# Performance work log

Measured on AMD Instinct MI355X. Metric: run time of the kernel, lower is better.

## Reference

```python
import jax, jax.numpy as jnp
import numpy as np

B, S, D, H, M = 4, 4096, 768, 12, 256
Dh = D // H
EPS_KERNEL = 1e-4
LN_EPS = 1e-5


def setup_inputs() -> dict:
    key = jax.random.key(0)
    ks = jax.random.split(key, 18)
    w = lambda k, sh: jax.random.normal(k, sh, jnp.float32) * 0.02
    return {
        "x": jax.random.normal(ks[0], (B, S, D), jnp.float32),
        # FAVOR+ random projection (performer uses orthogonal gaussian; gaussian here, same math)
        "proj": jax.random.normal(ks[1], (M, Dh), jnp.float32),
        "wq": w(ks[2], (D, D)), "bq": jnp.zeros((D,), jnp.float32),
        "wk": w(ks[3], (D, D)), "bk": jnp.zeros((D,), jnp.float32),
        "wv": w(ks[4], (D, D)), "bv": jnp.zeros((D,), jnp.float32),
        "wo": w(ks[5], (D, D)), "bo": jnp.zeros((D,), jnp.float32),
        "ln1_g": jnp.ones((D,), jnp.float32), "ln1_b": jnp.zeros((D,), jnp.float32),
        "ln2_g": jnp.ones((D,), jnp.float32), "ln2_b": jnp.zeros((D,), jnp.float32),
        "w1": w(ks[6], (4 * D, D)), "b1": jnp.zeros((4 * D,), jnp.float32),
        "w2": w(ks[7], (D, 4 * D)), "b2": jnp.zeros((D,), jnp.float32),
    }


def layernorm(x, g, b):
    mu = x.mean(-1, keepdims=True)
    var = ((x - mu) ** 2).mean(-1, keepdims=True)
    return (x - mu) / jnp.sqrt(var + LN_EPS) * g + b


def softmax_features(data, proj, is_query):
    # FAVOR+ positive softmax kernel features (performer-pytorch softmax_kernel)
    norm = data.shape[-1] ** -0.25
    ratio = proj.shape[0] ** -0.5
    dd = jnp.einsum('bhnd,md->bhnm', data * norm, proj)       # [B,H,S,M]
    diag = (data ** 2).sum(-1, keepdims=True) * 0.5 * norm * norm
    if is_query:
        mx = jnp.max(dd, axis=-1, keepdims=True)
    else:
        mx = jnp.max(dd)
    return ratio * (jnp.exp(dd - diag - mx) + EPS_KERNEL)


def performer_block(x, proj, wq, bq, wk, bk, wv, bv, wo, bo,
                    ln1_g, ln1_b, ln2_g, ln2_b, w1, b1, w2, b2):
    h = layernorm(x, ln1_g, ln1_b)
    split = lambda t: t.reshape(B, S, H, Dh).transpose(0, 2, 1, 3)  # [B,H,S,Dh]
    q = split(h @ wq.T + bq)
    k = split(h @ wk.T + bk)
    v = split(h @ wv.T + bv)

    qp = softmax_features(q, proj, True)    # [B,H,S,M]
    kp = softmax_features(k, proj, False)   # [B,H,S,M]

    # non-causal linear attention
    k_sum = kp.sum(axis=2)                                   # [B,H,M]
    d_inv = 1.0 / jnp.einsum('bhnm,bhm->bhn', qp, k_sum)     # [B,H,S]
    ctx = jnp.einsum('bhnm,bhnd->bhmd', kp, v)               # [B,H,M,Dh]
    attn = jnp.einsum('bhnm,bhmd,bhn->bhnd', qp, ctx, d_inv) # [B,H,S,Dh]
    attn = attn.transpose(0, 2, 1, 3).reshape(B, S, D)
    x = x + attn @ wo.T + bo

    h2 = layernorm(x, ln2_g, ln2_b)
    h2 = jax.nn.gelu(h2 @ w1.T + b1, approximate=False)
    x = x + h2 @ w2.T + b2
    return x


def reference(x, proj, wq, bq, wk, bk, wv, bv, wo, bo,
              ln1_g, ln1_b, ln2_g, ln2_b, w1, b1, w2, b2):
    return performer_block(x, proj, wq, bq, wk, bk, wv, bv, wo, bo,
                           ln1_g, ln1_b, ln2_g, ln2_b, w1, b1, w2, b2)
```

## Files before the change

kernel.cpp:

```cpp
#include <hip/hip_runtime.h>
#include <math.h>

typedef __attribute__((ext_vector_type(8))) short bf16x8;
typedef __attribute__((ext_vector_type(4))) float f32x4;

__device__ __forceinline__ float b2f(unsigned short u) {
    return __uint_as_float(((unsigned)u) << 16);
}
__device__ __forceinline__ unsigned short f2b(float f) {
    unsigned u = __float_as_uint(f);
    u += 0x7FFF + ((u >> 16) & 1);
    return (unsigned short)(u >> 16);
}
__device__ __forceinline__ void up2(unsigned u, float& a, float& b) {
    a = __uint_as_float(u << 16);
    b = __uint_as_float(u & 0xffff0000u);
}
__device__ __forceinline__ float gelu_exact(float v) {
    return 0.5f * v * (1.0f + erff(v * 0.70710678118654752f));
}
__device__ __forceinline__ void atomicMaxFloat(float* addr, float val) {
    unsigned* ua = (unsigned*)addr;
    unsigned old = *ua;
    while (true) {
        float of = __uint_as_float(old);
        if (of >= val) break;
        unsigned assumed = old;
        old = atomicCAS(ua, assumed, __float_as_uint(val));
        if (old == assumed) break;
    }
}
__device__ __forceinline__ void gl_lds16(const unsigned short* g, unsigned short* lds) {
    __builtin_amdgcn_global_load_lds((const __attribute__((address_space(1))) unsigned int*)g,
                                     (__attribute__((address_space(3))) unsigned int*)lds, 16, 0, 0);
}

__global__ void init_kernel(float* ksum, float* kmax) {
    int i = blockIdx.x * 256 + threadIdx.x;
    if (i < 48 * 256) ksum[i] = 0.0f;
    if (i == 0) *kmax = -3.0e38f;
}

__global__ __launch_bounds__(256)
void cvt_qkvp(const float* __restrict__ wq, const float* __restrict__ wk, const float* __restrict__ wv,
              const float* __restrict__ prj, unsigned short* __restrict__ wdst,
              unsigned short* __restrict__ pdst) {
    int i4 = (blockIdx.x * 256 + threadIdx.x) * 4;
    const float* s; unsigned short* d; int off;
    if (i4 < 1769472) { s = (i4 < 589824) ? wq : (i4 < 1179648 ? wk : wv);
        off = (i4 < 589824) ? i4 : (i4 < 1179648 ? i4 - 589824 : i4 - 1179648);
        d = wdst + i4; }
    else { s = prj; off = i4 - 1769472; d = pdst + off; }
    float4 v = *(const float4*)&s[off];
    ushort4 o; o.x = f2b(v.x); o.y = f2b(v.y); o.z = f2b(v.z); o.w = f2b(v.w);
    *(ushort4*)d = o;
}
__global__ __launch_bounds__(256)
void cvt_ow12(const float* __restrict__ wo, const float* __restrict__ w1, const float* __restrict__ w2,
              unsigned short* __restrict__ dst) {
    int i4 = (blockIdx.x * 256 + threadIdx.x) * 4;
    const float* s; int off;
    if (i4 < 589824) { s = wo; off = i4; }
    else if (i4 < 2949120) { s = w1; off = i4 - 589824; }
    else { s = w2; off = i4 - 2949120; }
    float4 v = *(const float4*)&s[off];
    ushort4 o; o.x = f2b(v.x); o.y = f2b(v.y); o.z = f2b(v.z); o.w = f2b(v.w);
    *(ushort4*)&dst[i4] = o;
}

template <bool IN_F32>
__global__ __launch_bounds__(256)
void ln_kernel(const void* __restrict__ Xv, const float* __restrict__ G,
               const float* __restrict__ Bb, unsigned short* __restrict__ OUT) {
    int row = blockIdx.x, t = threadIdx.x, wave = t >> 6, lane = t & 63;
    __shared__ float red[4];
    float x0, x1, x2;
    if constexpr (IN_F32) {
        const float* xr = (const float*)Xv + (size_t)row * 768;
        x0 = xr[t]; x1 = xr[t + 256]; x2 = xr[t + 512];
    } else {
        const unsigned short* xr = (const unsigned short*)Xv + (size_t)row * 768;
        x0 = b2f(xr[t]); x1 = b2f(xr[t + 256]); x2 = b2f(xr[t + 512]);
    }
    float s = x0 + x1 + x2;
#pragma unroll
    for (int d = 32; d; d >>= 1) s += __shfl_xor(s, d, 64);
    if (lane == 0) red[wave] = s;
    __syncthreads();
    float mean = (red[0] + red[1] + red[2] + red[3]) * (1.0f / 768.0f);
    __syncthreads();
    float d0 = x0 - mean, d1 = x1 - mean, d2 = x2 - mean;
    float s2 = d0 * d0 + d1 * d1 + d2 * d2;
#pragma unroll
    for (int d = 32; d; d >>= 1) s2 += __shfl_xor(s2, d, 64);
    if (lane == 0) red[wave] = s2;
    __syncthreads();
    float var = (red[0] + red[1] + red[2] + red[3]) * (1.0f / 768.0f);
    float inv = rsqrtf(var + 1e-5f);
    size_t base = (size_t)row * 768;
    OUT[base + t]       = f2b(d0 * inv * G[t]       + Bb[t]);
    OUT[base + t + 256] = f2b(d1 * inv * G[t + 256] + Bb[t + 256]);
    OUT[base + t + 512] = f2b(d2 * inv * G[t + 512] + Bb[t + 512]);
}

template <int EPI, bool R_F32, bool C_F32>
__global__ __launch_bounds__(512, 2)
void gemm_bt_256(const unsigned short* __restrict__ A, const unsigned short* __restrict__ Bm,
                 const float* __restrict__ bias, const void* __restrict__ R,
                 void* __restrict__ C, int N, int K, float alpha) {
    __shared__ unsigned short sA[2][256 * 64];
    __shared__ unsigned short sB[2][256 * 64];
    const int t = threadIdx.x;
    const int wave = t >> 6, lane = t & 63, quad = lane >> 4, l16 = lane & 15;
    const int nwg = gridDim.x * gridDim.y;
    int flat = blockIdx.y * gridDim.x + blockIdx.x;
    int q = nwg >> 3, r = nwg & 7;
    int xcd = flat & 7, idx = flat >> 3;
    int swz = (xcd < r ? xcd * (q + 1) : r * (q + 1) + (xcd - r) * q) + idx;
    const int m0 = (swz / gridDim.x) * 256;
    const int n0 = (swz % gridDim.x) * 256;
    const int wm = (wave >> 2) * 128, wn = (wave & 3) * 64;
    const int srow = t >> 3;
    const int scol = ((t & 7) ^ (srow & 7)) << 3;
    const unsigned short* gA = &A[(size_t)(m0 + srow) * K + scol];
    const unsigned short* gB = &Bm[(size_t)(n0 + srow) * K + scol];
    const size_t rstep = (size_t)64 * K;
    unsigned short* ldA0 = &sA[0][wave * 512];
    unsigned short* ldB0 = &sB[0][wave * 512];
    unsigned short* ldA1 = &sA[1][wave * 512];
    unsigned short* ldB1 = &sB[1][wave * 512];
    const int k0off = ((quad ^ (l16 & 7)) & 7) << 3;
    const int k1off = (((4 | quad) ^ (l16 & 7)) & 7) << 3;
    f32x4 acc[8][4] = {};
    const int nt = K >> 6;
#pragma unroll
    for (int u = 0; u < 4; ++u) {
        gl_lds16(gA + u * rstep, ldA0 + u * 4096);
        gl_lds16(gB + u * rstep, ldB0 + u * 4096);
    }
    __syncthreads();
    int cur = 0;
    for (int it = 0; it < nt; ++it) {
        if (it + 1 < nt) {
            const size_t kt = (size_t)(it + 1) << 6;
            unsigned short* dA = cur ? ldA0 : ldA1;
            unsigned short* dB = cur ? ldB0 : ldB1;
#pragma unroll
            for (int u = 0; u < 4; ++u) {
                gl_lds16(gA + u * rstep + kt, dA + u * 4096);
                gl_lds16(gB + u * rstep + kt, dB + u * 4096);
            }
        }
        const unsigned short* bufA = cur ? &sA[1][0] : &sA[0][0];
        const unsigned short* bufB = cur ? &sB[1][0] : &sB[0][0];
#pragma unroll
        for (int ks = 0; ks < 2; ++ks) {
            const int koff = ks ? k1off : k0off;
            bf16x8 bfr[4];
#pragma unroll
            for (int j = 0; j < 4; ++j)
                bfr[j] = *(const bf16x8*)&bufB[(wn + j * 16 + l16) * 64 + koff];
#pragma unroll
            for (int i = 0; i < 8; ++i) {
                bf16x8 af = *(const bf16x8*)&bufA[(wm + i * 16 + l16) * 64 + koff];
#pragma unroll
                for (int j = 0; j < 4; ++j)
                    acc[i][j] = __builtin_amdgcn_mfma_f32_16x16x32_bf16(af, bfr[j], acc[i][j], 0, 0, 0);
            }
        }
        __syncthreads();
        cur ^= 1;
    }
    if constexpr (EPI == 3) {
#pragma unroll
        for (int i = 0; i < 8; ++i) {
            int rowb = m0 + wm + i * 16 + quad * 4;
            int b_ = rowb >> 12, sbase = rowb & 4095;
#pragma unroll
            for (int j = 0; j < 4; ++j) {
                int col = n0 + wn + j * 16 + l16;
                float bs = bias[col];
                ushort4 o;
                o.x = f2b(acc[i][j][0] + bs);
                o.y = f2b(acc[i][j][1] + bs);
                o.z = f2b(acc[i][j][2] + bs);
                o.w = f2b(acc[i][j][3] + bs);
                size_t dst = (((size_t)b_ * 12 + (col >> 6)) * 64 + (col & 63)) * 4096 + sbase;
                *(ushort4*)&((unsigned short*)C)[dst] = o;
            }
        }
        return;
    }
#pragma unroll
    for (int i = 0; i < 8; ++i) {
        int rowb = m0 + wm + i * 16 + quad * 4;
#pragma unroll
        for (int j = 0; j < 4; ++j) {
            int col = n0 + wn + j * 16 + l16;
            float bs = bias[col];
#pragma unroll
            for (int r4 = 0; r4 < 4; ++r4) {
                size_t idx = (size_t)(rowb + r4) * N + col;
                float v = acc[i][j][r4] + bs;
                if constexpr (EPI == 0) v *= alpha;
                if constexpr (EPI == 1) {
                    if constexpr (R_F32) v += ((const float*)R)[idx];
                    else                 v += b2f(((const unsigned short*)R)[idx]);
                }
                if constexpr (EPI == 2) v = gelu_exact(v);
                if constexpr (C_F32) ((float*)C)[idx] = v;
                else                 ((unsigned short*)C)[idx] = f2b(v);
            }
        }
    }
}

__global__ __launch_bounds__(512, 2)
void gemm_qkv(const unsigned short* __restrict__ A, const unsigned short* __restrict__ Bm,
              const float* __restrict__ BQ, const float* __restrict__ BK,
              const float* __restrict__ BV, unsigned short* __restrict__ Cq,
              unsigned short* __restrict__ Ck, unsigned short* __restrict__ VT, float alpha) {
    const int K = 768;
    __shared__ unsigned short sA[2][256 * 64];
    __shared__ unsigned short sB[2][256 * 64];
    const int t = threadIdx.x;
    const int wave = t >> 6, lane = t & 63, quad = lane >> 4, l16 = lane & 15;
    const int nwg = gridDim.x * gridDim.y;
    int flat = blockIdx.y * gridDim.x + blockIdx.x;
    int q = nwg >> 3, r = nwg & 7;
    int xcd = flat & 7, idx = flat >> 3;
    int swz = (xcd < r ? xcd * (q + 1) : r * (q + 1) + (xcd - r) * q) + idx;
    const int m0 = (swz / gridDim.x) * 256;
    const int n0 = (swz % gridDim.x) * 256;
    const int wm = (wave >> 2) * 128, wn = (wave & 3) * 64;
    const int srow = t >> 3;
    const int scol = ((t & 7) ^ (srow & 7)) << 3;
    const unsigned short* gA = &A[(size_t)(m0 + srow) * K + scol];
    const unsigned short* gB = &Bm[(size_t)(n0 + srow) * K + scol];
    const size_t rstep = (size_t)64 * K;
    unsigned short* ldA0 = &sA[0][wave * 512];
    unsigned short* ldB0 = &sB[0][wave * 512];
    unsigned short* ldA1 = &sA[1][wave * 512];
    unsigned short* ldB1 = &sB[1][wave * 512];
    const int k0off = ((quad ^ (l16 & 7)) & 7) << 3;
    const int k1off = (((4 | quad) ^ (l16 & 7)) & 7) << 3;
    f32x4 acc[8][4] = {};
    const int nt = K >> 6;
#pragma unroll
    for (int u = 0; u < 4; ++u) {
        gl_lds16(gA + u * rstep, ldA0 + u * 4096);
        gl_lds16(gB + u * rstep, ldB0 + u * 4096);
    }
    __syncthreads();
    int cur = 0;
    for (int it = 0; it < nt; ++it) {
        if (it + 1 < nt) {
            const size_t kt = (size_t)(it + 1) << 6;
            unsigned short* dA = cur ? ldA0 : ldA1;
            unsigned short* dB = cur ? ldB0 : ldB1;
#pragma unroll
            for (int u = 0; u < 4; ++u) {
                gl_lds16(gA + u * rstep + kt, dA + u * 4096);
                gl_lds16(gB + u * rstep + kt, dB + u * 4096);
            }
        }
        const unsigned short* bufA = cur ? &sA[1][0] : &sA[0][0];
        const unsigned short* bufB = cur ? &sB[1][0] : &sB[0][0];
#pragma unroll
        for (int ks = 0; ks < 2; ++ks) {
            const int koff = ks ? k1off : k0off;
            bf16x8 bfr[4];
#pragma unroll
            for (int j = 0; j < 4; ++j)
                bfr[j] = *(const bf16x8*)&bufB[(wn + j * 16 + l16) * 64 + koff];
#pragma unroll
            for (int i = 0; i < 8; ++i) {
                bf16x8 af = *(const bf16x8*)&bufA[(wm + i * 16 + l16) * 64 + koff];
#pragma unroll
                for (int j = 0; j < 4; ++j)
                    acc[i][j] = __builtin_amdgcn_mfma_f32_16x16x32_bf16(af, bfr[j], acc[i][j], 0, 0, 0);
            }
        }
        __syncthreads();
        cur ^= 1;
    }
    const int seg = n0 / 768;
    const int nbase = n0 - seg * 768;
    const float* bias = (seg == 0) ? BQ : (seg == 1 ? BK : BV);
    if (seg == 2) {
#pragma unroll
        for (int i = 0; i < 8; ++i) {
            int rowb = m0 + wm + i * 16 + quad * 4;
            int b_ = rowb >> 12, sbase = rowb & 4095;
#pragma unroll
            for (int j = 0; j < 4; ++j) {
                int col = nbase + wn + j * 16 + l16;
                float bs = bias[col];
                ushort4 o;
                o.x = f2b(acc[i][j][0] + bs);
                o.y = f2b(acc[i][j][1] + bs);
                o.z = f2b(acc[i][j][2] + bs);
                o.w = f2b(acc[i][j][3] + bs);
                size_t dst = (((size_t)b_ * 12 + (col >> 6)) * 64 + (col & 63)) * 4096 + sbase;
                *(ushort4*)&VT[dst] = o;
            }
        }
    } else {
        unsigned short* Cn = (seg == 0) ? Cq : Ck;
#pragma unroll
        for (int i = 0; i < 8; ++i) {
            int rowb = m0 + wm + i * 16 + quad * 4;
#pragma unroll
            for (int j = 0; j < 4; ++j) {
                int col = nbase + wn + j * 16 + l16;
                float bs = bias[col];
#pragma unroll
                for (int r4 = 0; r4 < 4; ++r4) {
                    size_t idxo = (size_t)(rowb + r4) * 768 + col;
                    Cn[idxo] = f2b((acc[i][j][r4] + bs) * alpha);
                }
            }
        }
    }
}

template <int MODE>
__global__ __launch_bounds__(256)
void feat_kernel(const unsigned short* __restrict__ Q, const unsigned short* __restrict__ P,
                 unsigned short* __restrict__ OUTP, float* __restrict__ kmaxp,
                 float* __restrict__ ksump) {
    __shared__ unsigned short sQ[64 * 64];
    __shared__ unsigned short sP[256 * 64];
    __shared__ float sDiag[64];
    __shared__ float sRed[4];
    int t = threadIdx.x, wave = t >> 6, lane = t & 63, quad = lane >> 4, l16 = lane & 15;
    int bh = blockIdx.y, bq = bh / 12, hh = bh % 12;
    int s0 = blockIdx.x * 64;
    size_t rowbase = (size_t)bq * 4096 + s0;
#pragma unroll
    for (int u = 0; u < 2; ++u) {
        int L = u * 256 + t, row = L >> 3, c8 = (L & 7) * 8;
        *(uint4*)&sQ[row * 64 + c8] = *(const uint4*)&Q[(rowbase + row) * 768 + hh * 64 + c8];
    }
#pragma unroll
    for (int u = 0; u < 8; ++u) {
        int L = u * 256 + t, row = L >> 3, c8 = (L & 7) * 8;
        *(uint4*)&sP[row * 64 + c8] = *(const uint4*)&P[(size_t)row * 64 + c8];
    }
    __syncthreads();
    if (MODE != 1 && t < 64) {
        float d = 0.0f;
        for (int c = 0; c < 64; ++c) { float f = b2f(sQ[t * 64 + c]); d += f * f; }
        sDiag[t] = 0.5f * d;
    }
    f32x4 acc[4][4] = {};
#pragma unroll
    for (int ks = 0; ks < 2; ++ks) {
        bf16x8 af[4], bfr[4];
#pragma unroll
        for (int i = 0; i < 4; ++i) af[i] = *(const bf16x8*)&sQ[(i * 16 + l16) * 64 + ks * 32 + quad * 8];
#pragma unroll
        for (int j = 0; j < 4; ++j) bfr[j] = *(const bf16x8*)&sP[(wave * 64 + j * 16 + l16) * 64 + ks * 32 + quad * 8];
#pragma unroll
        for (int i = 0; i < 4; ++i)
#pragma unroll
            for (int j = 0; j < 4; ++j)
                acc[i][j] = __builtin_amdgcn_mfma_f32_16x16x32_bf16(af[i], bfr[j], acc[i][j], 0, 0, 0);
    }
    if constexpr (MODE == 1) {
        float m = -3.0e38f;
#pragma unroll
        for (int i = 0; i < 4; ++i)
#pragma unroll
            for (int j = 0; j < 4; ++j)
#pragma unroll
                for (int r = 0; r < 4; ++r) m = fmaxf(m, acc[i][j][r]);
#pragma unroll
        for (int d = 1; d < 64; d <<= 1) m = fmaxf(m, __shfl_xor(m, d, 64));
        if (lane == 0) sRed[wave] = m;
        __syncthreads();
        if (t == 0) atomicMaxFloat(kmaxp, fmaxf(fmaxf(sRed[0], sRed[1]), fmaxf(sRed[2], sRed[3])));
        return;
    } else {
        __syncthreads();
        float mx_k = *kmaxp;
        float csum[4] = {0.0f, 0.0f, 0.0f, 0.0f};
#pragma unroll
        for (int i = 0; i < 4; ++i)
#pragma unroll
            for (int j = 0; j < 4; ++j) {
                int col = wave * 64 + j * 16 + l16;
                ushort4 o;
#pragma unroll
                for (int r = 0; r < 4; ++r) {
                    int row = i * 16 + quad * 4 + r;
                    float v = 0.0625f * (expf(acc[i][j][r] - sDiag[row] - mx_k) + 1e-4f);
                    csum[j] += v;
                    (&o.x)[r] = f2b(v);
                }
                *(ushort4*)&OUTP[((size_t)bh * 256 + col) * 4096 + s0 + i * 16 + quad * 4] = o;
            }
#pragma unroll
        for (int j = 0; j < 4; ++j) {
            csum[j] += __shfl_xor(csum[j], 16, 64);
            csum[j] += __shfl_xor(csum[j], 32, 64);
        }
        if (quad == 0)
#pragma unroll
            for (int j = 0; j < 4; ++j)
                atomicAdd(&ksump[bh * 256 + wave * 64 + j * 16 + l16], csum[j]);
    }
}

__global__ __launch_bounds__(256)
void ctx_gemm(const unsigned short* __restrict__ KPT, const unsigned short* __restrict__ VT,
              float* __restrict__ part) {
    __shared__ unsigned short sV[2][64 * 32];
    __shared__ unsigned short sK[2][128 * 32];
    const int t = threadIdx.x;
    const int wave = t >> 6, lane = t & 63, quad = lane >> 4, l16 = lane & 15;
    const int bh = blockIdx.y;
    const int sc = blockIdx.x >> 1, mh = blockIdx.x & 1;
    const int m0 = mh * 128;
    const int k0 = sc * 512;
    const int srow = t >> 2;
    const int scol = ((t & 3) ^ (srow & 3)) << 3;
    const unsigned short* gv  = &VT [((size_t)bh * 64 + srow) * 4096 + k0 + scol];
    const unsigned short* gk0 = &KPT[((size_t)bh * 256 + m0 + srow) * 4096 + k0 + scol];
    const unsigned short* gk1 = &KPT[((size_t)bh * 256 + m0 + 64 + srow) * 4096 + k0 + scol];
    const int ldsoff = wave * 512;
    const int sw = ((quad ^ l16) & 3) << 3;
    f32x4 acc[4][2] = {};
    gl_lds16(gv,  &sV[0][ldsoff]);
    gl_lds16(gk0, &sK[0][ldsoff]);
    gl_lds16(gk1, &sK[0][2048 + ldsoff]);
    __syncthreads();
    int cur = 0;
    for (int it = 0; it < 16; ++it) {
        if (it + 1 < 16) {
            const int kt = (it + 1) << 5;
            gl_lds16(gv + kt,  &sV[cur ^ 1][ldsoff]);
            gl_lds16(gk0 + kt, &sK[cur ^ 1][ldsoff]);
            gl_lds16(gk1 + kt, &sK[cur ^ 1][2048 + ldsoff]);
        }
        bf16x8 af[4], bfr[2];
#pragma unroll
        for (int i = 0; i < 4; ++i) af[i] = *(const bf16x8*)&sV[cur][(i * 16 + l16) * 32 + sw];
#pragma unroll
        for (int j = 0; j < 2; ++j) bfr[j] = *(const bf16x8*)&sK[cur][(wave * 32 + j * 16 + l16) * 32 + sw];
#pragma unroll
        for (int i = 0; i < 4; ++i)
#pragma unroll
            for (int j = 0; j < 2; ++j)
                acc[i][j] = __builtin_amdgcn_mfma_f32_16x16x32_bf16(af[i], bfr[j], acc[i][j], 0, 0, 0);
        __syncthreads();
        cur ^= 1;
    }
    float* base = part + ((size_t)(sc * 48 + bh) * 64) * 256;
#pragma unroll
    for (int i = 0; i < 4; ++i)
#pragma unroll
        for (int r = 0; r < 4; ++r) {
            int d = i * 16 + quad * 4 + r;
#pragma unroll
            for (int j = 0; j < 2; ++j) {
                int m = m0 + wave * 32 + j * 16 + l16;
                base[(size_t)d * 256 + m] = acc[i][j][r];
            }
        }
}

__global__ __launch_bounds__(256)
void ctx_reduce(const float* __restrict__ part, unsigned short* __restrict__ ctxb) {
    size_t i = (size_t)blockIdx.x * 256 + threadIdx.x;
    float s = 0.0f;
#pragma unroll
    for (int c = 0; c < 8; ++c) s += part[(size_t)c * 786432 + i];
    ctxb[i] = f2b(s);
}

__global__ __launch_bounds__(256)
void feat_attn(const unsigned short* __restrict__ Q, const unsigned short* __restrict__ P,
               const unsigned short* __restrict__ CTX, const float* __restrict__ ksump,
               unsigned short* __restrict__ ATT) {
    __shared__ unsigned short sQ[64 * 64];
    __shared__ unsigned short sPQ[256 * 64];
    __shared__ unsigned short sCtx[64 * 256];
    __shared__ float sDiag[64];
    __shared__ float sRed[256];
    __shared__ float sWred[256];
    __shared__ float sKs[256];
    __shared__ float sDinv[64];
    int t = threadIdx.x, wave = t >> 6, lane = t & 63, quad = lane >> 4, l16 = lane & 15;
    int bh = blockIdx.y, bq = bh / 12, hh = bh % 12;
    int s0 = blockIdx.x * 64;
    size_t rowbase = (size_t)bq * 4096 + s0;
#pragma unroll
    for (int u = 0; u < 2; ++u) {
        int L = u * 256 + t, row = L >> 3, c8 = (L & 7) * 8;
        *(uint4*)&sQ[row * 64 + c8] = *(const uint4*)&Q[(rowbase + row) * 768 + hh * 64 + c8];
    }
#pragma unroll
    for (int u = 0; u < 8; ++u) {
        int L = u * 256 + t, row = L >> 3, c8 = (L & 7) * 8;
        *(uint4*)&sPQ[row * 64 + c8] = *(const uint4*)&P[(size_t)row * 64 + c8];
    }
#pragma unroll
    for (int u = 0; u < 8; ++u) {
        int L = u * 256 + t, d = L >> 5, m8 = L & 31;
        int m8s = (m8 & 28) | ((m8 ^ d) & 3);
        *(uint4*)&sCtx[d * 256 + m8s * 8] = *(const uint4*)&CTX[(size_t)bh * 16384 + d * 256 + m8 * 8];
    }
    sKs[t] = ksump[bh * 256 + t];
    __syncthreads();
    if (t < 64) {
        float d = 0.0f;
        for (int c = 0; c < 64; ++c) { float f = b2f(sQ[t * 64 + c]); d += f * f; }
        sDiag[t] = 0.5f * d;
    }
    f32x4 acc[4][4] = {};
#pragma unroll
    for (int ks = 0; ks < 2; ++ks) {
        bf16x8 af[4], bfr[4];
#pragma unroll
        for (int i = 0; i < 4; ++i) af[i] = *(const bf16x8*)&sQ[(i * 16 + l16) * 64 + ks * 32 + quad * 8];
#pragma unroll
        for (int j = 0; j < 4; ++j) bfr[j] = *(const bf16x8*)&sPQ[(wave * 64 + j * 16 + l16) * 64 + ks * 32 + quad * 8];
#pragma unroll
        for (int i = 0; i < 4; ++i)
#pragma unroll
            for (int j = 0; j < 4; ++j)
                acc[i][j] = __builtin_amdgcn_mfma_f32_16x16x32_bf16(af[i], bfr[j], acc[i][j], 0, 0, 0);
    }
#pragma unroll
    for (int i = 0; i < 4; ++i)
#pragma unroll
        for (int r = 0; r < 4; ++r) {
            float m = fmaxf(fmaxf(acc[i][0][r], acc[i][1][r]), fmaxf(acc[i][2][r], acc[i][3][r]));
#pragma unroll
            for (int d = 1; d < 16; d <<= 1) m = fmaxf(m, __shfl_xor(m, d, 64));
            if (l16 == 0) sRed[wave * 64 + i * 16 + quad * 4 + r] = m;
        }
    __syncthreads();
    if (t < 64) sRed[t] = fmaxf(fmaxf(sRed[t], sRed[64 + t]), fmaxf(sRed[128 + t], sRed[192 + t]));
    __syncthreads();
#pragma unroll
    for (int i = 0; i < 4; ++i)
#pragma unroll
        for (int r = 0; r < 4; ++r) {
            int row = i * 16 + quad * 4 + r;
            float diag = sDiag[row], mx = sRed[row];
            float p = 0.0f;
#pragma unroll
            for (int j = 0; j < 4; ++j) {
                int col = wave * 64 + j * 16 + l16;
                float v = 0.0625f * (expf(acc[i][j][r] - diag - mx) + 1e-4f);
                int colp = (col & ~31) | ((((col >> 3) ^ row) & 3) << 3) | (col & 7);
                sPQ[row * 256 + colp] = f2b(v);
                p += v * sKs[col];
            }
#pragma unroll
            for (int d = 1; d < 16; d <<= 1) p += __shfl_xor(p, d, 64);
            if (l16 == 0) sWred[wave * 64 + row] = p;
        }
    __syncthreads();
    if (t < 64) sDinv[t] = 1.0f / (sWred[t] + sWred[64 + t] + sWred[128 + t] + sWred[192 + t]);
    __syncthreads();
    const int w16 = wave * 16;
    const int aswz = ((quad ^ (l16 & 3)) << 3);
    f32x4 acc2[4] = {};
    const unsigned short* qrow = &sPQ[(w16 + l16) * 256];
#pragma unroll
    for (int kt = 0; kt < 256; kt += 32) {
        bf16x8 af = *(const bf16x8*)&qrow[kt + aswz];
#pragma unroll
        for (int j = 0; j < 4; ++j) {
            bf16x8 bf = *(const bf16x8*)&sCtx[(j * 16 + l16) * 256 + kt + aswz];
            acc2[j] = __builtin_amdgcn_mfma_f32_16x16x32_bf16(af, bf, acc2[j], 0, 0, 0);
        }
    }
#pragma unroll
    for (int rr = 0; rr < 4; ++rr) {
        int sr = w16 + quad * 4 + rr;
        float dv = sDinv[sr];
        size_t obase = ((size_t)bq * 4096 + s0 + sr) * 768 + hh * 64;
#pragma unroll
        for (int j = 0; j < 4; ++j)
            ATT[obase + j * 16 + l16] = f2b(acc2[j][rr] * dv);
    }
}

extern "C" void kernel_launch(void* const* d_in, const int* in_sizes, int n_in,
                              void* d_out, int out_size, void* d_ws, size_t ws_size,
                              hipStream_t stream) {
    const float* X   = (const float*)d_in[0];
    const float* PRJ = (const float*)d_in[1];
    const float* WQ  = (const float*)d_in[2];
    const float* BQ  = (const float*)d_in[3];
    const float* WK  = (const float*)d_in[4];
    const float* BKb = (const float*)d_in[5];
    const float* WV  = (const float*)d_in[6];
    const float* BV  = (const float*)d_in[7];
    const float* WO  = (const float*)d_in[8];
    const float* BO  = (const float*)d_in[9];
    const float* G1  = (const float*)d_in[10];
    const float* Bn1 = (const float*)d_in[11];
    const float* G2  = (const float*)d_in[12];
    const float* Bn2 = (const float*)d_in[13];
    const float* W1  = (const float*)d_in[14];
    const float* Bf1 = (const float*)d_in[15];
    const float* W2  = (const float*)d_in[16];
    const float* Bf2 = (const float*)d_in[17];
    float* OUT = (float*)d_out;

    char* w = (char*)d_ws;
    const size_t SZ_ACT = (size_t)16384 * 768 * 2;
    unsigned short* hbuf  = (unsigned short*)(w);
    float*          part  = (float*)(w);
    unsigned short* qn    = (unsigned short*)(w + SZ_ACT);
    unsigned short* wow12 = (unsigned short*)(w + SZ_ACT);
    unsigned short* kn    = (unsigned short*)(w + 2 * SZ_ACT);
    unsigned short* x2    = (unsigned short*)(w + 2 * SZ_ACT);
    unsigned short* vtb   = (unsigned short*)(w + 3 * SZ_ACT);
    unsigned short* attn  = (unsigned short*)(w + 3 * SZ_ACT);
    unsigned short* wqkv  = (unsigned short*)(w + 4 * SZ_ACT);
    unsigned short* kpt   = (unsigned short*)(w + 4 * SZ_ACT);
    unsigned short* gmid  = kpt;
    char* tail = w + 4 * SZ_ACT + (size_t)100663296;
    unsigned short* prjb = (unsigned short*)(tail);
    unsigned short* ctxb = (unsigned short*)(tail + 32768);
    float* ksum = (float*)(tail + 32768 + 1572864);
    float* kmax = (float*)(tail + 32768 + 1572864 + 49152);

    unsigned short* w1b = wow12 + 589824;
    unsigned short* w2b = wow12 + 2949120;
    unsigned short* wob = wow12;

    const float NORM = 0.35355339059327373f;

    init_kernel<<<48, 256, 0, stream>>>(ksum, kmax);
    cvt_qkvp<<<1744, 256, 0, stream>>>(WQ, WK, WV, PRJ, wqkv, prjb);
    ln_kernel<true><<<16384, 256, 0, stream>>>(X, G1, Bn1, hbuf);
    gemm_qkv<<<dim3(9, 64), 512, 0, stream>>>(hbuf, wqkv, BQ, BKb, BV, qn, kn, vtb, NORM);
    feat_kernel<1><<<dim3(64, 48), 256, 0, stream>>>(kn, prjb, nullptr, kmax, ksum);
    feat_kernel<2><<<dim3(64, 48), 256, 0, stream>>>(kn, prjb, kpt, kmax, ksum);
    ctx_gemm<<<dim3(16, 48), 256, 0, stream>>>(kpt, vtb, part);
    ctx_reduce<<<3072, 256, 0, stream>>>(part, ctxb);
    feat_attn<<<dim3(64, 48), 256, 0, stream>>>(qn, prjb, ctxb, ksum, attn);
    cvt_ow12<<<5184, 256, 0, stream>>>(WO, W1, W2, wow12);
    gemm_bt_256<1, true, false><<<dim3(3, 64), 512, 0, stream>>>(attn, wob, BO, X, x2, 768, 768, 1.0f);
    ln_kernel<false><<<16384, 256, 0, stream>>>(x2, G2, Bn2, hbuf);
    gemm_bt_256<2, false, false><<<dim3(12, 64), 512, 0, stream>>>(hbuf, w1b, Bf1, nullptr, gmid, 3072, 768, 1.0f);
    gemm_bt_256<1, false, true><<<dim3(3, 64), 512, 0, stream>>>(gmid, w2b, Bf2, x2, OUT, 768, 3072, 1.0f);
}
```

Baseline: 686.1 us.

## Shrink GEMM tiles to 256x128 and use three-stage LDS pipeline

All dense GEMMs now use 256x128 output tiles (8 waves of 64x64) instead of 256x256, doubling grid size, so the 768-wide GEMMs launch 384 workgroups instead of 192. That count is better matched to the CU count. The K-loop moves from double buffering with two barriers per step to a triple-buffered ring. It prefetches two tiles ahead and uses explicit vmcnt waits plus a single s_barrier per iteration. The cost is more redundant A-tile loads from the narrower N tile, and reliance on hand-counted vmcnt values.

```diff
diff --git a/kernel.cpp b/kernel.cpp
--- a/kernel.cpp
+++ b/kernel.cpp
@@ -33,6 +33,10 @@
 __device__ __forceinline__ void gl_lds16(const unsigned short* g, unsigned short* lds) {
     __builtin_amdgcn_global_load_lds((const __attribute__((address_space(1))) unsigned int*)g,
                                      (__attribute__((address_space(3))) unsigned int*)lds, 16, 0, 0);
+}
+template <int N> __device__ __forceinline__ void wait_vm() {
+    if constexpr (N == 0) asm volatile("s_waitcnt vmcnt(0)" ::: "memory");
+    if constexpr (N == 6) asm volatile("s_waitcnt vmcnt(6)" ::: "memory");
 }
 
 __global__ void init_kernel(float* ksum, float* kmax) {
@@ -105,11 +109,11 @@
 
 template <int EPI, bool R_F32, bool C_F32>
 __global__ __launch_bounds__(512, 2)
-void gemm_bt_256(const unsigned short* __restrict__ A, const unsigned short* __restrict__ Bm,
-                 const float* __restrict__ bias, const void* __restrict__ R,
-                 void* __restrict__ C, int N, int K, float alpha) {
-    __shared__ unsigned short sA[2][256 * 64];
-    __shared__ unsigned short sB[2][256 * 64];
+void gemm_bt_r(const unsigned short* __restrict__ A, const unsigned short* __restrict__ Bm,
+               const float* __restrict__ bias, const void* __restrict__ R,
+               void* __restrict__ C, int N, int K, float alpha) {
+    __shared__ unsigned short sA[3][256 * 64];
+    __shared__ unsigned short sB[3][128 * 64];
     const int t = threadIdx.x;
     const int wave = t >> 6, lane = t & 63, quad = lane >> 4, l16 = lane & 15;
     const int nwg = gridDim.x * gridDim.y;
@@ -118,41 +122,40 @@
     int xcd = flat & 7, idx = flat >> 3;
     int swz = (xcd < r ? xcd * (q + 1) : r * (q + 1) + (xcd - r) * q) + idx;
     const int m0 = (swz / gridDim.x) * 256;
-    const int n0 = (swz % gridDim.x) * 256;
-    const int wm = (wave >> 2) * 128, wn = (wave & 3) * 64;
+    const int n0 = (swz % gridDim.x) * 128;
+    const int wm = (wave >> 1) * 64, wn = (wave & 1) * 64;
     const int srow = t >> 3;
     const int scol = ((t & 7) ^ (srow & 7)) << 3;
     const unsigned short* gA = &A[(size_t)(m0 + srow) * K + scol];
     const unsigned short* gB = &Bm[(size_t)(n0 + srow) * K + scol];
     const size_t rstep = (size_t)64 * K;
-    unsigned short* ldA0 = &sA[0][wave * 512];
-    unsigned short* ldB0 = &sB[0][wave * 512];
-    unsigned short* ldA1 = &sA[1][wave * 512];
-    unsigned short* ldB1 = &sB[1][wave * 512];
     const int k0off = ((quad ^ (l16 & 7)) & 7) << 3;
     const int k1off = (((4 | quad) ^ (l16 & 7)) & 7) << 3;
-    f32x4 acc[8][4] = {};
+    f32x4 acc[4][4] = {};
     const int nt = K >> 6;
-#pragma unroll
-    for (int u = 0; u < 4; ++u) {
-        gl_lds16(gA + u * rstep, ldA0 + u * 4096);
-        gl_lds16(gB + u * rstep, ldB0 + u * 4096);
-    }
-    __syncthreads();
-    int cur = 0;
+    auto STAGE = [&](int tile, int slot) {
+        const size_t kt = (size_t)tile << 6;
+        unsigned short* dA = &sA[slot][wave * 512];
+        unsigned short* dB = &sB[slot][wave * 512];
+        gl_lds16(gA + kt, dA);
+        gl_lds16(gA + rstep + kt, dA + 4096);
+        gl_lds16(gA + 2 * rstep + kt, dA + 8192);
+        gl_lds16(gA + 3 * rstep + kt, dA + 12288);
+        gl_lds16(gB + kt, dB);
+        gl_lds16(gB + rstep + kt, dB + 4096);
+    };
+    STAGE(0, 0);
+    STAGE(1, 1);
+    int slot = 0;
     for (int it = 0; it < nt; ++it) {
-        if (it + 1 < nt) {
-            const size_t kt = (size_t)(it + 1) << 6;
-            unsigned short* dA = cur ? ldA0 : ldA1;
-            unsigned short* dB = cur ? ldB0 : ldB1;
-#pragma unroll
-            for (int u = 0; u < 4; ++u) {
-                gl_lds16(gA + u * rstep + kt, dA + u * 4096);
-                gl_lds16(gB + u * rstep + kt, dB + u * 4096);
-            }
-        }
-        const unsigned short* bufA = cur ? &sA[1][0] : &sA[0][0];
-        const unsigned short* bufB = cur ? &sB[1][0] : &sB[0][0];
+        if (it < nt - 1) wait_vm<6>(); else wait_vm<0>();
+        __builtin_amdgcn_s_barrier();
+        if (it + 2 < nt) {
+            int s2 = slot + 2; if (s2 >= 3) s2 -= 3;
+            STAGE(it + 2, s2);
+        }
+        const unsigned short* bufA = sA[slot];
+        const unsigned short* bufB = sB[slot];
 #pragma unroll
         for (int ks = 0; ks < 2; ++ks) {
             const int koff = ks ? k1off : k0off;
@@ -161,19 +164,18 @@
             for (int j = 0; j < 4; ++j)
                 bfr[j] = *(const bf16x8*)&bufB[(wn + j * 16 + l16) * 64 + koff];
 #pragma unroll
-            for (int i = 0; i < 8; ++i) {
+            for (int i = 0; i < 4; ++i) {
                 bf16x8 af = *(const bf16x8*)&bufA[(wm + i * 16 + l16) * 64 + koff];
 #pragma unroll
                 for (int j = 0; j < 4; ++j)
                     acc[i][j] = __builtin_amdgcn_mfma_f32_16x16x32_bf16(af, bfr[j], acc[i][j], 0, 0, 0);
             }
         }
-        __syncthreads();
-        cur ^= 1;
+        if (++slot == 3) slot = 0;
     }
     if constexpr (EPI == 3) {
 #pragma unroll
-        for (int i = 0; i < 8; ++i) {
+        for (int i = 0; i < 4; ++i) {
             int rowb = m0 + wm + i * 16 + quad * 4;
             int b_ = rowb >> 12, sbase = rowb & 4095;
 #pragma unroll
@@ -192,7 +194,7 @@
         return;
     }
 #pragma unroll
-    for (int i = 0; i < 8; ++i) {
+    for (int i = 0; i < 4; ++i) {
         int rowb = m0 + wm + i * 16 + quad * 4;
 #pragma unroll
         for (int j = 0; j < 4; ++j) {
@@ -221,8 +223,8 @@
               const float* __restrict__ BV, unsigned short* __restrict__ Cq,
               unsigned short* __restrict__ Ck, unsigned short* __restrict__ VT, float alpha) {
     const int K = 768;
-    __shared__ unsigned short sA[2][256 * 64];
-    __shared__ unsigned short sB[2][256 * 64];
+    __shared__ unsigned short sA[3][256 * 64];
+    __shared__ unsigned short sB[3][128 * 64];
     const int t = threadIdx.x;
     const int wave = t >> 6, lane = t & 63, quad = lane >> 4, l16 = lane & 15;
     const int nwg = gridDim.x * gridDim.y;
@@ -231,41 +233,40 @@
     int xcd = flat & 7, idx = flat >> 3;
     int swz = (xcd < r ? xcd * (q + 1) : r * (q + 1) + (xcd - r) * q) + idx;
     const int m0 = (swz / gridDim.x) * 256;
-    const int n0 = (swz % gridDim.x) * 256;
-    const int wm = (wave >> 2) * 128, wn = (wave & 3) * 64;
+    const int n0 = (swz % gridDim.x) * 128;
+    const int wm = (wave >> 1) * 64, wn = (wave & 1) * 64;
     const int srow = t >> 3;
     const int scol = ((t & 7) ^ (srow & 7)) << 3;
     const unsigned short* gA = &A[(size_t)(m0 + srow) * K + scol];
     const unsigned short* gB = &Bm[(size_t)(n0 + srow) * K + scol];
     const size_t rstep = (size_t)64 * K;
-    unsigned short* ldA0 = &sA[0][wave * 512];
-    unsigned short* ldB0 = &sB[0][wave * 512];
-    unsigned short* ldA1 = &sA[1][wave * 512];
-    unsigned short* ldB1 = &sB[1][wave * 512];
     const int k0off = ((quad ^ (l16 & 7)) & 7) << 3;
     const int k1off = (((4 | quad) ^ (l16 & 7)) & 7) << 3;
-    f32x4 acc[8][4] = {};
+    f32x4 acc[4][4] = {};
     const int nt = K >> 6;
-#pragma unroll
-    for (int u = 0; u < 4; ++u) {
-        gl_lds16(gA + u * rstep, ldA0 + u * 4096);
-        gl_lds16(gB + u * rstep, ldB0 + u * 4096);
-    }
-    __syncthreads();
-    int cur = 0;
+    auto STAGE = [&](int tile, int slot) {
+        const size_t kt = (size_t)tile << 6;
+        unsigned short* dA = &sA[slot][wave * 512];
+        unsigned short* dB = &sB[slot][wave * 512];
+        gl_lds16(gA + kt, dA);
+        gl_lds16(gA + rstep + kt, dA + 4096);
+        gl_lds16(gA + 2 * rstep + kt, dA + 8192);
+        gl_lds16(gA + 3 * rstep + kt, dA + 12288);
+        gl_lds16(gB + kt, dB);
+        gl_lds16(gB + rstep + kt, dB + 4096);
+    };
+    STAGE(0, 0);
+    STAGE(1, 1);
+    int slot = 0;
     for (int it = 0; it < nt; ++it) {
-        if (it + 1 < nt) {
-            const size_t kt = (size_t)(it + 1) << 6;
-            unsigned short* dA = cur ? ldA0 : ldA1;
-            unsigned short* dB = cur ? ldB0 : ldB1;
-#pragma unroll
-            for (int u = 0; u < 4; ++u) {
-                gl_lds16(gA + u * rstep + kt, dA + u * 4096);
-                gl_lds16(gB + u * rstep + kt, dB + u * 4096);
-            }
-        }
-        const unsigned short* bufA = cur ? &sA[1][0] : &sA[0][0];
-        const unsigned short* bufB = cur ? &sB[1][0] : &sB[0][0];
+        if (it < nt - 1) wait_vm<6>(); else wait_vm<0>();
+        __builtin_amdgcn_s_barrier();
+        if (it + 2 < nt) {
+            int s2 = slot + 2; if (s2 >= 3) s2 -= 3;
+            STAGE(it + 2, s2);
+        }
+        const unsigned short* bufA = sA[slot];
+        const unsigned short* bufB = sB[slot];
 #pragma unroll
         for (int ks = 0; ks < 2; ++ks) {
             const int koff = ks ? k1off : k0off;
@@ -274,22 +275,21 @@
             for (int j = 0; j < 4; ++j)
                 bfr[j] = *(const bf16x8*)&bufB[(wn + j * 16 + l16) * 64 + koff];
 #pragma unroll
-            for (int i = 0; i < 8; ++i) {
+            for (int i = 0; i < 4; ++i) {
                 bf16x8 af = *(const bf16x8*)&bufA[(wm + i * 16 + l16) * 64 + koff];
 #pragma unroll
                 for (int j = 0; j < 4; ++j)
                     acc[i][j] = __builtin_amdgcn_mfma_f32_16x16x32_bf16(af, bfr[j], acc[i][j], 0, 0, 0);
             }
         }
-        __syncthreads();
-        cur ^= 1;
+        if (++slot == 3) slot = 0;
     }
     const int seg = n0 / 768;
     const int nbase = n0 - seg * 768;
     const float* bias = (seg == 0) ? BQ : (seg == 1 ? BK : BV);
     if (seg == 2) {
 #pragma unroll
-        for (int i = 0; i < 8; ++i) {
+        for (int i = 0; i < 4; ++i) {
             int rowb = m0 + wm + i * 16 + quad * 4;
             int b_ = rowb >> 12, sbase = rowb & 4095;
 #pragma unroll
@@ -308,7 +308,7 @@
     } else {
         unsigned short* Cn = (seg == 0) ? Cq : Ck;
 #pragma unroll
-        for (int i = 0; i < 8; ++i) {
+        for (int i = 0; i < 4; ++i) {
             int rowb = m0 + wm + i * 16 + quad * 4;
 #pragma unroll
             for (int j = 0; j < 4; ++j) {
@@ -641,15 +641,15 @@
     init_kernel<<<48, 256, 0, stream>>>(ksum, kmax);
     cvt_qkvp<<<1744, 256, 0, stream>>>(WQ, WK, WV, PRJ, wqkv, prjb);
     ln_kernel<true><<<16384, 256, 0, stream>>>(X, G1, Bn1, hbuf);
-    gemm_qkv<<<dim3(9, 64), 512, 0, stream>>>(hbuf, wqkv, BQ, BKb, BV, qn, kn, vtb, NORM);
+    gemm_qkv<<<dim3(18, 64), 512, 0, stream>>>(hbuf, wqkv, BQ, BKb, BV, qn, kn, vtb, NORM);
     feat_kernel<1><<<dim3(64, 48), 256, 0, stream>>>(kn, prjb, nullptr, kmax, ksum);
     feat_kernel<2><<<dim3(64, 48), 256, 0, stream>>>(kn, prjb, kpt, kmax, ksum);
     ctx_gemm<<<dim3(16, 48), 256, 0, stream>>>(kpt, vtb, part);
     ctx_reduce<<<3072, 256, 0, stream>>>(part, ctxb);
     feat_attn<<<dim3(64, 48), 256, 0, stream>>>(qn, prjb, ctxb, ksum, attn);
     cvt_ow12<<<5184, 256, 0, stream>>>(WO, W1, W2, wow12);
-    gemm_bt_256<1, true, false><<<dim3(3, 64), 512, 0, stream>>>(attn, wob, BO, X, x2, 768, 768, 1.0f);
+    gemm_bt_r<1, true, false><<<dim3(6, 64), 512, 0, stream>>>(attn, wob, BO, X, x2, 768, 768, 1.0f);
     ln_kernel<false><<<16384, 256, 0, stream>>>(x2, G2, Bn2, hbuf);
-    gemm_bt_256<2, false, false><<<dim3(12, 64), 512, 0, stream>>>(hbuf, w1b, Bf1, nullptr, gmid, 3072, 768, 1.0f);
-    gemm_bt_256<1, false, true><<<dim3(3, 64), 512, 0, stream>>>(gmid, w2b, Bf2, x2, OUT, 768, 3072, 1.0f);
-}
+    gemm_bt_r<2, false, false><<<dim3(24, 64), 512, 0, stream>>>(hbuf, w1b, Bf1, nullptr, gmid, 3072, 768, 1.0f);
+    gemm_bt_r<1, false, true><<<dim3(6, 64), 512, 0, stream>>>(gmid, w2b, Bf2, x2, OUT, 768, 3072, 1.0f);
+}
```

New measurement: 919.0 us. 1.34x slower.
